# Kernel tuning notes

Hardware: AMD Instinct MI355X
Metric: run time of the kernel (lower is better)

Reference implementation:

```python
import jax, jax.numpy as jnp
import numpy as np

B, CI, CO = 8, 32, 32
M1, M2 = 16, 16
H, W = 128, 128
TOTAL = M1 + M2 + M1 * M2  # 288


def setup_inputs() -> dict:
    key = jax.random.key(0)
    k1, k2, k3 = jax.random.split(key, 3)
    scale = 1.0 / (CI * CO)
    x = jax.random.normal(k1, (B, CI, H, W), dtype=jnp.float32)
    weight_real = scale * jax.random.uniform(k2, (CI, CO, TOTAL), dtype=jnp.float32)
    weight_imag = scale * jax.random.uniform(k3, (CI, CO, TOTAL), dtype=jnp.float32)
    return {"x": x, "weight_real": weight_real, "weight_imag": weight_imag}


def reference(x, weight_real, weight_imag):
    w = (weight_real + 1j * weight_imag).astype(jnp.complex64)
    pole1 = w[:, :, :M1]                                   # [i,o,p]
    pole2 = w[:, :, M1:M1 + M2]                            # [i,o,q]
    residue = w[:, :, M1 + M2:].reshape(CI, CO, M1, M2)    # [i,o,p,q]

    Hh, Wd = x.shape[-2], x.shape[-1]
    ty = jnp.linspace(0.0, 1.0, Hh)   # grid along dim -2
    tx = jnp.linspace(0.0, 1.0, Wd)   # grid along dim -1
    dty = ty[1] - ty[0]
    dtx = tx[1] - tx[0]

    # FFT (torch default norm='backward': no scaling on forward)
    alpha = jnp.fft.fft2(x, axes=(-2, -1))[:, :, :M1, :M2]  # [b,i,f,g] complex

    lam1 = (jnp.fft.fftfreq(Hh, dty) * (2.0 * np.pi) * 1j)[:M1].astype(jnp.complex64)  # [f]
    lam2 = (jnp.fft.fftfreq(Wd, dtx) * (2.0 * np.pi) * 1j)[:M2].astype(jnp.complex64)  # [g]

    # pole-residue transfer function Hw[f,g,i,o,p,q] = res[i,o,p,q] / ((lam1[f]-pole1[i,o,p]) * (lam2[g]-pole2[i,o,q]))
    d1 = lam1[:, None, None, None] - pole1[None]  # [f,i,o,p]
    d2 = lam2[:, None, None, None] - pole2[None]  # [g,i,o,q]
    Hw = residue[None, None] / (d1[:, None, :, :, :, None] * d2[None, :, :, :, None, :])  # [f,g,i,o,p,q]

    # contractions matching torch einsums 'biox,oxikpq->bkox' and '->bkpq'
    or1 = jnp.einsum('bifg,fgiopq->bofg', alpha, Hw)  # [b,o,f,g]
    or2 = jnp.einsum('bifg,fgiopq->bopq', alpha, Hw)  # [b,o,p,q]

    # ifft2 with zero-padding of modes to full (H, W), norm='backward' (1/(HW) on inverse)
    x1 = jnp.real(jnp.fft.ifft2(or1, s=(Hh, Wd), axes=(-2, -1)))

    # time-domain pole exponentials
    e1 = jnp.exp(pole1[..., None] * ty.astype(jnp.complex64))  # [i,o,p,z]
    e2 = jnp.exp(pole2[..., None] * tx.astype(jnp.complex64))  # [i,o,q,x]
    # x2[b,o,z,x] = sum_{i,p,q} or2[b,o,p,q] e1[i,o,p,z] e2[i,o,q,x]  (avoids 6D [i,o,p,q,H,W] intermediate)
    tmp = jnp.einsum('bopq,iopz->bioqz', or2, e1)          # [b,i,o,q,z]
    x2 = jnp.real(jnp.einsum('bioqz,ioqx->bozx', tmp, e2)) / (Hh * Wd)

    return x1 + x2
```

## Files before the change

kernel.cpp:

```cpp
#include <hip/hip_runtime.h>

#define TOT 288
#define W1C 6.2340979026f

typedef short short8 __attribute__((ext_vector_type(8)));
typedef float f32x4 __attribute__((ext_vector_type(4)));
typedef unsigned short u16;
typedef u16 u16x8 __attribute__((ext_vector_type(8)));

__device__ __forceinline__ u16 f2bf(float f) {
    unsigned u = __builtin_bit_cast(unsigned, f);
    u += 0x7fffu + ((u >> 16) & 1u);
    return (u16)(u >> 16);
}
__device__ __forceinline__ float2 cmul(float2 a, float2 b) {
    return make_float2(a.x * b.x - a.y * b.y, a.x * b.y + a.y * b.x);
}
__device__ __forceinline__ float2 cadd(float2 a, float2 b) {
    return make_float2(a.x + b.x, a.y + b.y);
}
__device__ __forceinline__ float2 cfma(float2 a, float2 b, float2 c) {
    return make_float2(c.x + a.x * b.x - a.y * b.y, c.y + a.x * b.y + a.y * b.x);
}
__device__ __forceinline__ void chi_basis(int f, float2 c[3]) {
    if (f == 0) {
        c[0] = make_float2(1.f, 0.f); c[1] = make_float2(0.f, 0.f); c[2] = make_float2(0.f, 0.f);
    } else {
        float w = W1C * (float)f;
        float iw = 1.0f / w;
        c[0] = make_float2(0.f, 0.f);
        c[1] = make_float2(0.f, -iw);
        c[2] = make_float2(-iw * iw, 0.f);
    }
}


__global__ __launch_bounds__(256) void k_pre(const float* __restrict__ x,
                                             const float* __restrict__ wr,
                                             const float* __restrict__ wi,
                                             float2* __restrict__ Sv,
                                             float2* __restrict__ Dv,
                                             u16* __restrict__ fA, u16* __restrict__ fB,
                                             float2* __restrict__ alpha) {
    __shared__ float sm[4352];
    const int bid = blockIdx.x;
    const int t = threadIdx.x;

    if (bid < 256) {
        float* T1r = sm;
        float* T1i = sm + 2112;
        int bi = bid;
        const float* xp = x + (size_t)bi * 16384;
        int xcol = t & 127;
        int f0 = (t >> 7) * 8;
        float ar[8], ai[8], rcr[8], rci[8], str[8], sti[8];
#pragma unroll
        for (int j = 0; j < 8; ++j) {
            ar[j] = 0.f; ai[j] = 0.f;
            rcr[j] = 1.f; rci[j] = 0.f;
            float s, c;
            sincosf(0.049087385212340517f * (float)(f0 + j), &s, &c);
            str[j] = c; sti[j] = -s;
        }
        for (int y = 0; y < 128; ++y) {
            float xv = xp[y * 128 + xcol];
#pragma unroll
            for (int j = 0; j < 8; ++j) {
                ar[j] += rcr[j] * xv;
                ai[j] += rci[j] * xv;
                float nr = rcr[j] * str[j] - rci[j] * sti[j];
                rci[j] = rcr[j] * sti[j] + rci[j] * str[j];
                rcr[j] = nr;
            }
        }
#pragma unroll
        for (int j = 0; j < 8; ++j) {
            T1r[(f0 + j) * 132 + xcol] = ar[j];
            T1i[(f0 + j) * 132 + xcol] = ai[j];
        }
        __syncthreads();

        int g = t & 15, f = t >> 4;
        float sr = 0.f, si = 0.f;
        float c2r = 1.f, c2i = 0.f, s2r, s2i;
        {
            float s, c;
            sincosf(0.049087385212340517f * (float)g, &s, &c);
            s2r = c; s2i = -s;
        }
        for (int xx = 0; xx < 128; ++xx) {
            float trv = T1r[f * 132 + xx], tiv = T1i[f * 132 + xx];
            sr += trv * c2r - tiv * c2i;
            si += trv * c2i + tiv * c2r;
            float nr = c2r * s2r - c2i * s2i;
            c2i = c2r * s2i + c2i * s2r;
            c2r = nr;
        }
        alpha[bi * 256 + t] = make_float2(sr, si);
    } else if (bid < 288) {
        int o = bid - 256;
        int p = t >> 4, q = t & 15;
        float Sr[4][4], Si[4][4];
#pragma unroll
        for (int n = 0; n < 4; ++n)
#pragma unroll
            for (int m = 0; m < 4; ++m) { Sr[n][m] = 0.f; Si[n][m] = 0.f; }
        for (int i = 0; i < 32; ++i) {
            int io = i * 32 + o;
            float p1r = wr[io * TOT + p],      p1i = wi[io * TOT + p];
            float p2r = wr[io * TOT + 16 + q], p2i = wi[io * TOT + 16 + q];
            float a1r[4], a1i[4], a2r[4], a2i[4];
            a1r[0] = 1.f; a1i[0] = 0.f;
            a2r[0] = 1.f; a2i[0] = 0.f;
#pragma unroll
            for (int n = 1; n < 4; ++n) {
                a1r[n] = a1r[n-1] * p1r - a1i[n-1] * p1i;
                a1i[n] = a1r[n-1] * p1i + a1i[n-1] * p1r;
                a2r[n] = a2r[n-1] * p2r - a2i[n-1] * p2i;
                a2i[n] = a2r[n-1] * p2i + a2i[n-1] * p2r;
            }
#pragma unroll
            for (int n = 0; n < 4; ++n)
#pragma unroll
                for (int m = 0; m < 4; ++m) {
                    Sr[n][m] += a1r[n] * a2r[m] - a1i[n] * a2i[m];
                    Si[n][m] += a1r[n] * a2i[m] + a1i[n] * a2r[m];
                }
        }
        const float facs[4] = {1.f, 1.f, 0.5f, 0.16666666666f};
        const float isz = 1.0f / 16384.0f;
#pragma unroll
        for (int n = 0; n < 4; ++n)
#pragma unroll
            for (int m = 0; m < 4; ++m) {
                float fac = facs[n] * facs[m] * isz;
                Sv[(size_t)(o * 16 + n * 4 + m) * 256 + t] =
                    make_float2(Sr[n][m] * fac, Si[n][m] * fac);
            }
    } else if (bid < 416) {
        int base = (bid - 288) * 8;
        int wp = t >> 6, l = t & 63;
#pragma unroll
        for (int s = 0; s < 2; ++s) {
            int io = base + wp * 2 + s;
            float2 Dacc[9];
#pragma unroll
            for (int jk = 0; jk < 9; ++jk) Dacc[jk] = make_float2(0.f, 0.f);
#pragma unroll
            for (int k = 0; k < 4; ++k) {
                int e = l + 64 * k;
                int p = e >> 4, q = e & 15;
                float2 p1 = make_float2(wr[io * TOT + p], wi[io * TOT + p]);
                float i1 = 1.0f / (p1.x * p1.x + p1.y * p1.y);
                float2 phip = make_float2(-p1.x * i1, p1.y * i1);
                float2 p2 = make_float2(wr[io * TOT + 16 + q], wi[io * TOT + 16 + q]);
                float i2 = 1.0f / (p2.x * p2.x + p2.y * p2.y);
                float2 psip = make_float2(-p2.x * i2, p2.y * i2);
                float2 R = make_float2(wr[io * TOT + 32 + e], wi[io * TOT + 32 + e]);
                float2 Rphi[3] = {cmul(R, phip), R, cmul(R, p1)};
                float2 psi[3] = {psip, make_float2(1.f, 0.f), p2};
#pragma unroll
                for (int j = 0; j < 3; ++j)
#pragma unroll
                    for (int k2 = 0; k2 < 3; ++k2)
                        Dacc[j * 3 + k2] = cfma(Rphi[j], psi[k2], Dacc[j * 3 + k2]);
            }
#pragma unroll
            for (int jk = 0; jk < 9; ++jk) {
#pragma unroll
                for (int m = 32; m >= 1; m >>= 1) {
                    Dacc[jk].x += __shfl_xor(Dacc[jk].x, m);
                    Dacc[jk].y += __shfl_xor(Dacc[jk].y, m);
                }
            }
            if (l == 0) {
                int o = io & 31, i = io >> 5;
#pragma unroll
                for (int jk = 0; jk < 9; ++jk)
                    Dv[(size_t)(o * 32 + i) * 9 + jk] = Dacc[jk];
            }
        }
    } else {
        for (int cidx = t; cidx < 1024; cidx += 256) {
            int tbl = cidx >> 9, mc = cidx & 511;
            int z = mc >> 2, cp = mc & 3;
            int c = cp ^ ((z >> 1) & 3);
            u16x8 v;
#pragma unroll
            for (int j = 0; j < 8; ++j) {
                int k = c * 8 + j, f = k & 15, part = k >> 4;
                float th = 0.049087385212340517f * (float)((f * z) & 127);
                float s, cs;
                sincosf(th, &s, &cs);
                float val = part ? ((tbl == 0) ? s : -s) : cs;
                v[j] = f2bf(val);
            }
            u16* dst = (tbl == 0 ? fA : fB) + mc * 8;
            *(u16x8*)dst = v;
        }
    }
}

__global__ __launch_bounds__(256) void k_mid(const float* __restrict__ wr,
                                             const float* __restrict__ wi,
                                             const float2* __restrict__ alpha,
                                             const float2* __restrict__ Dv,
                                             float2* __restrict__ or1,
                                             float2* __restrict__ or2p) {
    __shared__ float2 CaL[4][9];
    const int bid = blockIdx.x;
    const int t = threadIdx.x;

    if (bid < 256) {
        int bo = bid;
        int b = bo >> 5, o = bo & 31;
        int f = t >> 4, g = t & 15;
        float2 X[3], Xi[3];
        chi_basis(f, X);
        chi_basis(g, Xi);
        float2 B[9];
#pragma unroll
        for (int j = 0; j < 3; ++j)
#pragma unroll
            for (int k = 0; k < 3; ++k)
                B[j * 3 + k] = cmul(X[j], Xi[k]);
        float2 acc = make_float2(0.f, 0.f);
        for (int i = 0; i < 32; ++i) {
            const float2* Dp = Dv + (size_t)(o * 32 + i) * 9;
            float2 s1v = make_float2(0.f, 0.f);
#pragma unroll
            for (int jk = 0; jk < 9; ++jk)
                s1v = cfma(Dp[jk], B[jk], s1v);
            float2 a = alpha[(b * 32 + i) * 256 + t];
            acc = cfma(a, s1v, acc);
        }
        or1[bo * 256 + t] = acc;
    } else {
        int idx = bid - 256;
        int bo = idx & 255;
        int ic = idx >> 8;
        int b = bo >> 5, o = bo & 31;
        int wp = t >> 6, l = t & 63;
        {
            int i = ic * 4 + wp;
            float2 Ca[9];
#pragma unroll
            for (int jk = 0; jk < 9; ++jk) Ca[jk] = make_float2(0.f, 0.f);
#pragma unroll
            for (int k = 0; k < 4; ++k) {
                int e = l + 64 * k;
                int f = e >> 4, g = e & 15;
                float2 X[3], Xi[3];
                chi_basis(f, X);
                chi_basis(g, Xi);
                float2 a = alpha[(b * 32 + i) * 256 + e];
                float2 aX[3] = {cmul(a, X[0]), cmul(a, X[1]), cmul(a, X[2])};
#pragma unroll
                for (int j = 0; j < 3; ++j)
#pragma unroll
                    for (int k2 = 0; k2 < 3; ++k2)
                        Ca[j * 3 + k2] = cfma(aX[j], Xi[k2], Ca[j * 3 + k2]);
            }
#pragma unroll
            for (int jk = 0; jk < 9; ++jk) {
#pragma unroll
                for (int m = 32; m >= 1; m >>= 1) {
                    Ca[jk].x += __shfl_xor(Ca[jk].x, m);
                    Ca[jk].y += __shfl_xor(Ca[jk].y, m);
                }
            }
            if (l == 0) {
#pragma unroll
                for (int jk = 0; jk < 9; ++jk) CaL[wp][jk] = Ca[jk];
            }
        }
        __syncthreads();

        int p_ = t >> 4, q_ = t & 15;
        float2 acc = make_float2(0.f, 0.f);
#pragma unroll
        for (int ii = 0; ii < 4; ++ii) {
            int i = ic * 4 + ii;
            int io = i * 32 + o;
            float2 p1 = make_float2(wr[io * TOT + p_], wi[io * TOT + p_]);
            float i1 = 1.0f / (p1.x * p1.x + p1.y * p1.y);
            float2 phip = make_float2(-p1.x * i1, p1.y * i1);
            float2 p2 = make_float2(wr[io * TOT + 16 + q_], wi[io * TOT + 16 + q_]);
            float i2 = 1.0f / (p2.x * p2.x + p2.y * p2.y);
            float2 psip = make_float2(-p2.x * i2, p2.y * i2);
            float2 R = make_float2(wr[io * TOT + 32 + t], wi[io * TOT + 32 + t]);
            float2 c0 = CaL[ii][0], c1 = CaL[ii][1], c2 = CaL[ii][2];
            float2 c3 = CaL[ii][3], c4 = CaL[ii][4], c5 = CaL[ii][5];
            float2 c6 = CaL[ii][6], c7 = CaL[ii][7], c8 = CaL[ii][8];
            float2 col0 = cfma(c6, p1, cfma(c0, phip, c3));
            float2 col1 = cfma(c7, p1, cfma(c1, phip, c4));
            float2 col2 = cfma(c8, p1, cfma(c2, phip, c5));
            float2 T = cfma(col2, p2, cfma(col0, psip, col1));
            acc = cfma(R, T, acc);
        }
        or2p[(size_t)ic * 65536 + bo * 256 + t] = acc;
    }
}

__global__ __launch_bounds__(512, 4) void k_x12m(
        const float2* __restrict__ or1v,
        const float2* __restrict__ or2p,
        const float2* __restrict__ Sv,
        const u16* __restrict__ fA,
        const u16* __restrict__ fB,
        float* __restrict__ out) {
    __shared__ u16 EA[2048];
    __shared__ u16 EB[4096];
    __shared__ u16 GL[2048];
    __shared__ float2 SM1[256];
    __shared__ float2 SM2[256];
    __shared__ float CP[16];

    const int t = threadIdx.x;
    const int l = t & 63, w = t >> 6;
    const int bid = blockIdx.x;
    const int o = bid & 31, b = (bid >> 5) & 7, zh = bid >> 8;
    const int bo = b * 32 + o;
    const int q = l & 15, c4 = l >> 4, k0 = c4 * 8;

    for (int ch = w; ch < 12; ch += 8) {
        const u16* g;
        u16* d;
        if (ch < 4) { g = fA + zh * 2048 + ch * 512 + l * 8; d = &EA[ch * 512]; }
        else { g = fB + (ch - 4) * 512 + l * 8; d = &EB[(ch - 4) * 512]; }
        __builtin_amdgcn_global_load_lds(
            (const __attribute__((address_space(1))) unsigned*)g,
            (__attribute__((address_space(3))) unsigned*)d, 16, 0, 0);
    }

    if (t < 256) {
        float sr = 0.f, si = 0.f;
#pragma unroll
        for (int ic = 0; ic < 8; ++ic) {
            float2 v = or2p[(size_t)ic * 65536 + bo * 256 + t];
            sr += v.x; si += v.y;
        }
        SM2[t] = make_float2(sr, si);
        SM1[t] = or1v[bo * 256 + t];
    }
    __syncthreads();

    {
        int gidx = t >> 5;
        int j = t & 31;
        const float2* Sg = Sv + (size_t)(o * 16 + gidx) * 256;
        float part = 0.f;
#pragma unroll
        for (int k = 0; k < 8; ++k) {
            int pq = j + 32 * k;
            float2 s = Sg[pq];
            float2 v = SM2[pq];
            part += v.x * s.x - v.y * s.y;
        }
#pragma unroll
        for (int msk = 16; msk >= 1; msk >>= 1)
            part += __shfl_xor(part, msk, 32);
        if (j == 0) CP[gidx] = part;
    }

    short8 mF0, mF1;
#pragma unroll
    for (int j = 0; j < 8; ++j) {
        int k = k0 + j, f = k & 15;
        float2 m1 = SM1[f * 16 + q];
        if (k < 16) { mF0[j] = (short)f2bf(m1.x); mF1[j] = (short)f2bf(m1.y); }
        else        { mF0[j] = (short)f2bf(-m1.y); mF1[j] = (short)f2bf(m1.x); }
    }
    const short8 bF = (w & 1) ? mF1 : mF0;

    const int zt_g = w >> 1;
    const int zL_g = zt_g * 16 + q;
    const int cw_g = c4 ^ ((zL_g >> 1) & 3);
    const int kk_g = q + ((w & 1) << 4);
    const int x_ = w * 16 + q;
    const int cb_ = c4 ^ ((x_ >> 1) & 3);

    {
        short8 aG = *(const short8*)&EA[zL_g * 32 + cw_g * 8];
        f32x4 g = (f32x4){0.f, 0.f, 0.f, 0.f};
        g = __builtin_amdgcn_mfma_f32_16x16x32_bf16(aG, bF, g, 0, 0, 0);
#pragma unroll
        for (int r = 0; r < 4; ++r) {
            int zz = zt_g * 16 + c4 * 4 + r;
            int cc = (kk_g >> 3) ^ ((zz >> 1) & 3);
            GL[zz * 32 + cc * 8 + (kk_g & 7)] = f2bf(g[r]);
        }
    }
    __syncthreads();

    f32x4 acc[4];
    {
        short8 bf = *(const short8*)&EB[x_ * 32 + cb_ * 8];
#pragma unroll
        for (int zt = 0; zt < 4; ++zt) {
            int zL = zt * 16 + q;
            int ca = c4 ^ ((zL >> 1) & 3);
            short8 af = *(const short8*)&GL[zL * 32 + ca * 8];
            f32x4 a = (f32x4){0.f, 0.f, 0.f, 0.f};
            acc[zt] = __builtin_amdgcn_mfma_f32_16x16x32_bf16(af, bf, a, 0, 0, 0);
        }
    }

    const float sc = 1.0f / 16384.0f;
    const float tx = (float)x_ * 0.007874015748031496f;
    float R[4];
#pragma unroll
    for (int n = 0; n < 4; ++n)
        R[n] = ((CP[n * 4 + 3] * tx + CP[n * 4 + 2]) * tx + CP[n * 4 + 1]) * tx + CP[n * 4 + 0];
#pragma unroll
    for (int zt = 0; zt < 4; ++zt) {
        int zbase = zh * 64 + zt * 16 + c4 * 4;
        f32x4 a = acc[zt];
#pragma unroll
        for (int r = 0; r < 4; ++r) {
            float tz = (float)(zbase + r) * 0.007874015748031496f;
            float poly = ((R[3] * tz + R[2]) * tz + R[1]) * tz + R[0];
            out[(size_t)bo * 16384 + (zbase + r) * 128 + x_] = a[r] * sc + poly;
        }
    }
}

extern "C" void kernel_launch(void* const* d_in, const int* in_sizes, int n_in,
                              void* d_out, int out_size, void* d_ws, size_t ws_size,
                              hipStream_t stream) {
    const float* x  = (const float*)d_in[0];
    const float* wr = (const float*)d_in[1];
    const float* wi = (const float*)d_in[2];
    float* out = (float*)d_out;
    float* ws = (float*)d_ws;

    float2* alpha = (float2*)(ws + 256);
    float2* Dv    = (float2*)(ws + 1179904);
    float2* or1   = (float2*)(ws + 1704192);
    float2* Sv    = (float2*)(ws + 1966336);
    u16*    fA    = (u16*)(ws + 6160640);
    u16*    fB    = (u16*)(ws + 6162688);
    float2* or2p  = (float2*)(ws + 6164736);

    hipLaunchKernelGGL(k_pre,  dim3(417),  dim3(256), 0, stream,
                       x, wr, wi, Sv, Dv, fA, fB, alpha);
    hipLaunchKernelGGL(k_mid,  dim3(2304), dim3(256), 0, stream,
                       wr, wi, alpha, Dv, or1, or2p);
    hipLaunchKernelGGL(k_x12m, dim3(512),  dim3(512), 0, stream,
                       or1, or2p, Sv, fA, fB, out);
}
```

Before: 52.00 us.

## Split truncated-DFT stage into a wide column pass and a separate row-pass kernel

The first DFT pass over rows now gives each thread one frequency per column and spreads the work over 2048 blocks instead of 256, so one thread no longer carries eight accumulator sets. The intermediate moves from shared memory to a global workspace buffer. A new kernel then does the second pass over columns, splitting each row into two halves with separate twiddle chains to shorten the dependency chain. The aim is more parallelism and shorter serial recurrences in the alpha computation, at the cost of an extra kernel launch, a global round-trip for the intermediate, and re-reading x per frequency pair.

```diff
diff --git a/kernel.cpp b/kernel.cpp
--- a/kernel.cpp
+++ b/kernel.cpp
@@ -15,9 +15,6 @@
 }
 __device__ __forceinline__ float2 cmul(float2 a, float2 b) {
     return make_float2(a.x * b.x - a.y * b.y, a.x * b.y + a.y * b.x);
-}
-__device__ __forceinline__ float2 cadd(float2 a, float2 b) {
-    return make_float2(a.x + b.x, a.y + b.y);
 }
 __device__ __forceinline__ float2 cfma(float2 a, float2 b, float2 c) {
     return make_float2(c.x + a.x * b.x - a.y * b.y, c.y + a.x * b.y + a.y * b.x);
@@ -38,67 +35,34 @@
 __global__ __launch_bounds__(256) void k_pre(const float* __restrict__ x,
                                              const float* __restrict__ wr,
                                              const float* __restrict__ wi,
+                                             float2* __restrict__ T1,
                                              float2* __restrict__ Sv,
                                              float2* __restrict__ Dv,
-                                             u16* __restrict__ fA, u16* __restrict__ fB,
-                                             float2* __restrict__ alpha) {
-    __shared__ float sm[4352];
+                                             u16* __restrict__ fA, u16* __restrict__ fB) {
     const int bid = blockIdx.x;
     const int t = threadIdx.x;
 
-    if (bid < 256) {
-        float* T1r = sm;
-        float* T1i = sm + 2112;
-        int bi = bid;
-        const float* xp = x + (size_t)bi * 16384;
-        int xcol = t & 127;
-        int f0 = (t >> 7) * 8;
-        float ar[8], ai[8], rcr[8], rci[8], str[8], sti[8];
-#pragma unroll
-        for (int j = 0; j < 8; ++j) {
-            ar[j] = 0.f; ai[j] = 0.f;
-            rcr[j] = 1.f; rci[j] = 0.f;
-            float s, c;
-            sincosf(0.049087385212340517f * (float)(f0 + j), &s, &c);
-            str[j] = c; sti[j] = -s;
-        }
+    if (bid < 2048) {
+        int bi = bid >> 3;
+        int f = (bid & 7) * 2 + (t >> 7);
+        int xc = t & 127;
+        const float* xp = x + (size_t)bi * 16384 + xc;
+        float sr, ss;
+        sincosf(0.049087385212340517f * (float)f, &ss, &sr);
+        float cr = 1.f, ci = 0.f;
+        float ar = 0.f, ai = 0.f;
+#pragma unroll 4
         for (int y = 0; y < 128; ++y) {
-            float xv = xp[y * 128 + xcol];
-#pragma unroll
-            for (int j = 0; j < 8; ++j) {
-                ar[j] += rcr[j] * xv;
-                ai[j] += rci[j] * xv;
-                float nr = rcr[j] * str[j] - rci[j] * sti[j];
-                rci[j] = rcr[j] * sti[j] + rci[j] * str[j];
-                rcr[j] = nr;
-            }
-        }
-#pragma unroll
-        for (int j = 0; j < 8; ++j) {
-            T1r[(f0 + j) * 132 + xcol] = ar[j];
-            T1i[(f0 + j) * 132 + xcol] = ai[j];
-        }
-        __syncthreads();
-
-        int g = t & 15, f = t >> 4;
-        float sr = 0.f, si = 0.f;
-        float c2r = 1.f, c2i = 0.f, s2r, s2i;
-        {
-            float s, c;
-            sincosf(0.049087385212340517f * (float)g, &s, &c);
-            s2r = c; s2i = -s;
-        }
-        for (int xx = 0; xx < 128; ++xx) {
-            float trv = T1r[f * 132 + xx], tiv = T1i[f * 132 + xx];
-            sr += trv * c2r - tiv * c2i;
-            si += trv * c2i + tiv * c2r;
-            float nr = c2r * s2r - c2i * s2i;
-            c2i = c2r * s2i + c2i * s2r;
-            c2r = nr;
-        }
-        alpha[bi * 256 + t] = make_float2(sr, si);
-    } else if (bid < 288) {
-        int o = bid - 256;
+            float xv = xp[y * 128];
+            ar += cr * xv;
+            ai += ci * xv;
+            float nr = cr * sr + ci * ss;
+            ci = ci * sr - cr * ss;
+            cr = nr;
+        }
+        T1[(size_t)(bi * 16 + f) * 128 + xc] = make_float2(ar, ai);
+    } else if (bid < 2080) {
+        int o = bid - 2048;
         int p = t >> 4, q = t & 15;
         float Sr[4][4], Si[4][4];
 #pragma unroll
@@ -137,8 +101,8 @@
                 Sv[(size_t)(o * 16 + n * 4 + m) * 256 + t] =
                     make_float2(Sr[n][m] * fac, Si[n][m] * fac);
             }
-    } else if (bid < 416) {
-        int base = (bid - 288) * 8;
+    } else if (bid < 2208) {
+        int base = (bid - 2080) * 8;
         int wp = t >> 6, l = t & 63;
 #pragma unroll
         for (int s = 0; s < 2; ++s) {
@@ -199,6 +163,36 @@
             *(u16x8*)dst = v;
         }
     }
+}
+
+__global__ __launch_bounds__(256) void k_alpha2(const float2* __restrict__ T1,
+                                                float2* __restrict__ alpha) {
+    const int bi = blockIdx.x;
+    const int t = threadIdx.x;
+    const int f = t >> 4, g = t & 15;
+    const float2* tp = T1 + (size_t)(bi * 16 + f) * 128;
+
+    float sr, ss;
+    sincosf(0.049087385212340517f * (float)g, &ss, &sr);
+    float c0r = 1.f, c0i = 0.f;
+    float c1r = (g & 1) ? -1.f : 1.f, c1i = 0.f;
+    float a0r = 0.f, a0i = 0.f, a1r = 0.f, a1i = 0.f;
+#pragma unroll 4
+    for (int xx = 0; xx < 64; ++xx) {
+        float2 v0 = tp[xx];
+        float2 v1 = tp[xx + 64];
+        a0r += v0.x * c0r - v0.y * c0i;
+        a0i += v0.x * c0i + v0.y * c0r;
+        a1r += v1.x * c1r - v1.y * c1i;
+        a1i += v1.x * c1i + v1.y * c1r;
+        float n0 = c0r * sr + c0i * ss;
+        c0i = c0i * sr - c0r * ss;
+        c0r = n0;
+        float n1 = c1r * sr + c1i * ss;
+        c1i = c1i * sr - c1r * ss;
+        c1r = n1;
+    }
+    alpha[bi * 256 + t] = make_float2(a0r + a1r, a0i + a1i);
 }
 
 __global__ __launch_bounds__(256) void k_mid(const float* __restrict__ wr,
@@ -435,6 +429,7 @@
     float* ws = (float*)d_ws;
 
     float2* alpha = (float2*)(ws + 256);
+    float2* T1    = (float2*)(ws + 131328);
     float2* Dv    = (float2*)(ws + 1179904);
     float2* or1   = (float2*)(ws + 1704192);
     float2* Sv    = (float2*)(ws + 1966336);
@@ -442,10 +437,11 @@
     u16*    fB    = (u16*)(ws + 6162688);
     float2* or2p  = (float2*)(ws + 6164736);
 
-    hipLaunchKernelGGL(k_pre,  dim3(417),  dim3(256), 0, stream,
-                       x, wr, wi, Sv, Dv, fA, fB, alpha);
-    hipLaunchKernelGGL(k_mid,  dim3(2304), dim3(256), 0, stream,
+    hipLaunchKernelGGL(k_pre,    dim3(2209), dim3(256), 0, stream,
+                       x, wr, wi, T1, Sv, Dv, fA, fB);
+    hipLaunchKernelGGL(k_alpha2, dim3(256),  dim3(256), 0, stream, T1, alpha);
+    hipLaunchKernelGGL(k_mid,    dim3(2304), dim3(256), 0, stream,
                        wr, wi, alpha, Dv, or1, or2p);
-    hipLaunchKernelGGL(k_x12m, dim3(512),  dim3(512), 0, stream,
+    hipLaunchKernelGGL(k_x12m,   dim3(512),  dim3(512), 0, stream,
                        or1, or2p, Sv, fA, fB, out);
 }
```

Measured after the change: 67.56 us. 29.9% more time.
